# Performance work log

Measured on AMD Instinct MI355X. Metric: run time of the kernel, lower is better.

## Reference

```python
import jax, jax.numpy as jnp
import numpy as np

EPSILON = 0.01        # temperature
DIST_THRESH = 0.2
NUM_ITERS = 8         # sparse_rebalance_iters (== num_iters here)
TOPK = 64             # topk_support
NEG_INF = -1e9


def setup_inputs() -> dict:
    key = jax.random.key(0)
    k1, k2, k3 = jax.random.split(key, 3)
    B, N, M, D = 4, 4096, 4096, 128
    return {
        "source_feats": jax.random.normal(k1, (B, N, D), dtype=jnp.float32),
        "source_locs": jax.random.uniform(k2, (B, N, 2), dtype=jnp.float32),
        "target_locs": jax.random.uniform(k3, (B, M, 2), dtype=jnp.float32),
        "source_valid_mask": jnp.ones((B, N), dtype=bool),
        "target_valid_mask": jnp.ones((B, M), dtype=bool),
    }


def _sinkhorn_attn(source_locs, target_locs, source_valid_mask, target_valid_mask):
    # pairwise squared distances: [B, M, N]
    diff = target_locs[:, :, None, :] - source_locs[:, None, :, :]
    dist_sq = jnp.sum(diff * diff, axis=-1)
    log_k = -dist_sq / (EPSILON + 1e-8)
    valid = (dist_sq < DIST_THRESH ** 2)
    valid = valid & source_valid_mask[:, None, :] & target_valid_mask[:, :, None]

    B, M, N = valid.shape
    topk = min(TOPK, N)
    if topk < N:
        masked_log_k = jnp.where(valid, log_k, NEG_INF)
        _, topk_idx = jax.lax.top_k(masked_log_k, topk)  # [B, M, topk]
        support = jnp.zeros_like(valid).at[
            jnp.arange(B)[:, None, None], jnp.arange(M)[None, :, None], topk_idx
        ].set(True)
        valid = valid & support

    log_k = jnp.where(valid, log_k, NEG_INF)

    v = jnp.zeros((B, 1, N), dtype=log_k.dtype)
    u = jnp.zeros((B, M, 1), dtype=log_k.dtype)
    for _ in range(NUM_ITERS):
        u = -jax.nn.logsumexp(log_k + v, axis=2, keepdims=True)
        v = -jax.nn.logsumexp(log_k + u, axis=1, keepdims=True)
        v = jnp.where(source_valid_mask[:, None, :], v, 0.0)

    attn = jnp.exp(log_k + u + v)              # [B, M, N]
    has_source = valid.any(axis=-1, keepdims=True)  # [B, M, 1]
    return attn, has_source


def reference(source_feats, source_locs, target_locs, source_valid_mask, target_valid_mask):
    attn, has_source = _sinkhorn_attn(source_locs, target_locs,
                                      source_valid_mask, target_valid_mask)
    target_feats = jnp.einsum('bmn,bnd->bmd', attn, source_feats)
    target_feats = target_feats * target_valid_mask[:, :, None].astype(target_feats.dtype)
    target_feats = target_feats * has_source.astype(target_feats.dtype)
    return target_feats
```

## Files before the change

kernel.cpp:

```cpp
#include <hip/hip_runtime.h>
#include <math.h>

#define B 4
#define N 4096
#define M 4096
#define D 128
#define K 64
#define BT 256
#define WPB 4
#define RPW 4
#define CAP 768
#define CUTCAP 128
#define PC 128
#define EPS_DENOM 0.01000001f
#define THRESH2 0.04f
#define GC 16

__global__ __launch_bounds__(1024) void k_sort(const float* __restrict__ slocs,
        const float* __restrict__ tlocs,
        float4* __restrict__ sPack, float4* __restrict__ tPack,
        int* __restrict__ cellStart,
        int* __restrict__ colcnt, int* __restrict__ E, int* __restrict__ R,
        float* __restrict__ extraF, float* __restrict__ cs){
    __shared__ int hist[256], startS[256], fill[256], wtot[4];
    __shared__ float2 loc[N];
    __shared__ unsigned short scell[N];
    const int blk = blockIdx.x, tid = threadIdx.x;
    const bool tgt = blk >= B;
    const int b = tgt ? (blk - B) : blk;
    const int lane = tid & 63, w = tid >> 6;
    const float2* slp = (const float2*)((tgt ? tlocs : slocs) + (size_t)b * N * 2);
    float4* outPack = (tgt ? tPack : sPack) + (size_t)b * N;

    if (!tgt){
        for (int i = tid; i < N; i += 1024){
            colcnt[b * N + i] = 0;
            cs[b * N + i] = 1.0f;
        }
        if (b == 0){
            if (tid < B){ E[tid] = 0; R[tid] = 0; }
            if (tid < B * D) extraF[tid] = 0.f;
        }
    }

    if (tid < 256){ hist[tid] = 0; fill[tid] = 0; }
    __syncthreads();
    for (int i = tid; i < N; i += 1024){
        float2 p = slp[i];
        int cx = min(GC - 1, max(0, (int)(p.x * (float)GC)));
        int cy = min(GC - 1, max(0, (int)(p.y * (float)GC)));
        int cell = cy * GC + cx;
        loc[i] = p; scell[i] = (unsigned short)cell;
        atomicAdd(&hist[cell], 1);
    }
    __syncthreads();
    int hv = (tid < 256) ? hist[tid] : 0;
    int pre = hv;
    #pragma unroll
    for (int o = 1; o < 64; o <<= 1){ int t2 = __shfl_up(pre, o, 64); if (lane >= o) pre += t2; }
    if (tid < 256 && lane == 63) wtot[w] = pre;
    __syncthreads();
    if (tid < 256){
        int off = 0;
        for (int i = 0; i < w; ++i) off += wtot[i];
        int st = off + pre - hv;
        startS[tid] = st;
        if (!tgt) cellStart[b * 257 + tid] = st;
    }
    if (!tgt && tid == 0) cellStart[b * 257 + 256] = N;
    __syncthreads();
    for (int i = tid; i < N; i += 1024){
        int cell = scell[i];
        int pos = startS[cell] + atomicAdd(&fill[cell], 1);
        float2 p = loc[i];
        outPack[pos] = make_float4(p.x, p.y, __int_as_float(i), 0.f);
    }
}

__global__ __launch_bounds__(BT, 4) void k_build(const float4* __restrict__ sPack,
        const int* __restrict__ cellStart, const float4* __restrict__ tPack,
        float* __restrict__ elkA, int* __restrict__ idxA, int* __restrict__ cnt,
        int* __restrict__ colcnt, float* __restrict__ cscElk, int* __restrict__ cscRow,
        int* __restrict__ R){
    __shared__ int cs[257];
    __shared__ float cd2[WPB][CAP];
    __shared__ int   cn [WPB][CAP];
    __shared__ int   hist[WPB][64];
    __shared__ float cutd[WPB][CUTCAP];
    __shared__ int   cutn[WPB][CUTCAP];

    const int bid  = blockIdx.x;
    const int sb   = (bid & 7) * 128 + (bid >> 3);
    const int b    = sb >> 8;
    const int s00  = (sb & 255) * (WPB * RPW);
    const int tid  = threadIdx.x;
    const int w    = tid >> 6;
    const int lane = tid & 63;
    const unsigned long long pmask = (lane == 0) ? 0ull : ((1ull << lane) - 1);
    const float4* sp = sPack + (size_t)b * N;
    const float4* tp = tPack + (size_t)b * M;

    for (int i = tid; i < 257; i += BT) cs[i] = cellStart[b * 257 + i];
    __syncthreads();

    for (int r = 0; r < RPW; ++r){
        const int srt   = s00 + w * RPW + r;
        const float4 t  = tp[srt];
        const float tx  = t.x;
        const float ty  = t.y;
        const int m     = __float_as_int(t.z);
        const int rowid = b * M + m;

        hist[w][lane] = 0;

        const int cy0 = max(0, (int)floorf((ty - 0.2f) * (float)GC - 0.001f));
        const int cy1 = min(GC - 1, (int)floorf((ty + 0.2f) * (float)GC + 0.001f));

        int c = 0;
        for (int cy = cy0; cy <= cy1; ++cy){
            float rowLo = cy * 0.0625f, rowHi = rowLo + 0.0625f;
            float dymin = fmaxf(0.f, fmaxf(rowLo - ty, ty - rowHi));
            float dxm = sqrtf(fmaxf(THRESH2 - dymin * dymin + 1e-5f, 0.f));
            int cx0 = max(0, (int)floorf((tx - dxm) * (float)GC - 0.001f));
            int cx1 = min(GC - 1, (int)floorf((tx + dxm) * (float)GC + 0.001f));
            int s = cs[cy * GC + cx0], e = cs[cy * GC + cx1 + 1];
            for (int j0 = s; j0 < e; j0 += 64){
                int j = j0 + lane;
                bool valid = j < e;
                float d2 = 1e9f; int n = 0;
                if (valid){
                    float4 q = sp[j];
                    float dx = __fsub_rn(tx, q.x);
                    float dy = __fsub_rn(ty, q.y);
                    d2 = __fadd_rn(__fmul_rn(dx, dx), __fmul_rn(dy, dy));
                    n = __float_as_int(q.z);
                }
                bool in = valid && (d2 < THRESH2);
                unsigned long long ml = __ballot(in);
                if (in){
                    int p = c + __popcll(ml & pmask);
                    if (p < CAP){ cd2[w][p] = d2; cn[w][p] = n; }
                    atomicAdd(&hist[w][min((int)(d2 * 1600.0f), 63)], 1);
                }
                c += __popcll(ml);
            }
        }
        const int ctot = min(c, CAP);

        int h = hist[w][lane];
        int pre = h;
        #pragma unroll
        for (int o = 1; o < 64; o <<= 1){
            int t2 = __shfl_up(pre, o, 64);
            if (lane >= o) pre += t2;
        }
        int cutB = 64, q = 0;
        if (c > K){
            unsigned long long ge = __ballot(pre >= K);
            int fb = __ffsll((long long)ge) - 1;
            cutB = fb;
            q = K - __shfl(pre - h, fb, 64);
        }

        int base = 0, cutc = 0;
        for (int i0 = 0; i0 < ctot; i0 += 64){
            int i = i0 + lane;
            bool valid = i < ctot;
            float d2 = 1e9f; int n = 0;
            if (valid){ d2 = cd2[w][i]; n = cn[w][i]; }
            int bk = valid ? min((int)(d2 * 1600.0f), 63) : 64;
            bool low = valid && (bk < cutB);
            unsigned long long ml = __ballot(low);
            if (low){
                int p = base + __popcll(ml & pmask);
                float e = expf(-(d2 / EPS_DENOM));
                elkA[(size_t)rowid * K + p] = e;
                idxA[(size_t)rowid * K + p] = n;
                int bn = b * N + n;
                int slot = atomicAdd(&colcnt[bn], 1);
                if (slot < PC){
                    cscElk[(size_t)bn * PC + slot] = e;
                    cscRow[(size_t)bn * PC + slot] = rowid;
                }
            }
            base += __popcll(ml);
            if (cutB < 64){
                bool eq = valid && (bk == cutB);
                unsigned long long me = __ballot(eq);
                if (eq){
                    int p = cutc + __popcll(me & pmask);
                    if (p < CUTCAP){ cutd[w][p] = d2; cutn[w][p] = n; }
                }
                cutc += __popcll(me);
            }
        }

        if (c > K){
            int cc = min(cutc, CUTCAP);
            for (int i0 = 0; i0 < CUTCAP; i0 += 64){
                int i = i0 + lane;
                bool sel = false; float d2i = 0.f; int ni = 0;
                if (i < cc){
                    d2i = cutd[w][i]; ni = cutn[w][i];
                    int rank = 0;
                    for (int j = 0; j < cc; ++j){
                        float dj = cutd[w][j]; int nj = cutn[w][j];
                        rank += (dj < d2i) || (dj == d2i && nj < ni);
                    }
                    sel = rank < q;
                }
                unsigned long long ms = __ballot(sel);
                if (sel){
                    int p = base + __popcll(ms & pmask);
                    float e = expf(-(d2i / EPS_DENOM));
                    elkA[(size_t)rowid * K + p] = e;
                    idxA[(size_t)rowid * K + p] = ni;
                    int bn = b * N + ni;
                    int slot = atomicAdd(&colcnt[bn], 1);
                    if (slot < PC){
                        cscElk[(size_t)bn * PC + slot] = e;
                        cscRow[(size_t)bn * PC + slot] = rowid;
                    }
                }
                base += __popcll(ms);
                if (i0 + 64 >= cc) break;
            }
            if (lane == 0) cnt[rowid] = K;
        } else {
            if (lane == 0){
                cnt[rowid] = c;
                if (c == 0) atomicAdd(&R[b], 1);
            }
        }
    }
}

__global__ __launch_bounds__(256) void k_prep(const int* __restrict__ colcnt,
        int* __restrict__ E, const float* __restrict__ feats, float* __restrict__ extraF){
    int t = blockIdx.x * blockDim.x + threadIdx.x;
    int lane = t & 63, b = t >> 12;
    int cc = colcnt[t];
    unsigned long long em = __ballot(cc == 0);
    if (lane == 0 && em) atomicAdd(&E[b], __popcll(em));
    if (cc == 0){
        for (int d = 0; d < D; ++d)
            atomicAdd(&extraF[b * D + d], feats[(size_t)t * D + d]);
    }
}

__global__ __launch_bounds__(256) void kA(const float* __restrict__ elkA,
        const int* __restrict__ idxA, const int* __restrict__ cnt,
        const float* __restrict__ cs, const int* __restrict__ E, float* __restrict__ eu){
    int t = blockIdx.x * blockDim.x + threadIdx.x;
    int W = t >> 6, lane = t & 63;
    for (int rr = 0; rr < 4; ++rr){
        int rid = W * 4 + rr;
        int b = rid >> 12;
        int c = cnt[rid];
        float s = 0.f;
        if (lane < c){
            int ix = (b << 12) + idxA[(size_t)rid * K + lane];
            s = elkA[(size_t)rid * K + lane] / cs[ix];
        }
        #pragma unroll
        for (int o = 32; o; o >>= 1) s += __shfl_xor(s, o, 64);
        int Eb = E[b];
        if (c == 0 && Eb == 0){
            if (lane == 0) eu[rid] = 0.f;
        } else {
            if (Eb > 0) s += (float)Eb;
            if (lane == 0) eu[rid] = 1.0f / s;
        }
    }
}

__global__ __launch_bounds__(256) void kB(const float* __restrict__ cscElk,
        const int* __restrict__ cscRow, const int* __restrict__ colcnt,
        const float* __restrict__ eu, const int* __restrict__ R, float* __restrict__ cs){
    int t = blockIdx.x * blockDim.x + threadIdx.x;
    int W = t >> 6, lane = t & 63;
    for (int rr = 0; rr < 4; ++rr){
        int cid = W * 4 + rr;
        int b = cid >> 12;
        int cc = min(colcnt[cid], PC);
        float s = 0.f;
        for (int p = lane; p < cc; p += 64)
            s += cscElk[(size_t)cid * PC + p] * eu[cscRow[(size_t)cid * PC + p]];
        #pragma unroll
        for (int o = 32; o; o >>= 1) s += __shfl_xor(s, o, 64);
        if (lane == 0)
            cs[cid] = s + (float)R[b];
    }
}

__global__ __launch_bounds__(128) void k_out(const float* __restrict__ feats,
        const float* __restrict__ elkA, const int* __restrict__ idxA,
        const int* __restrict__ cnt, const float* __restrict__ eu,
        const float* __restrict__ cs, const float* __restrict__ extraF,
        float* __restrict__ out){
    __shared__ float att[K];
    __shared__ int   sidx[K];
    int rid = blockIdx.x;
    int b = rid >> 12;
    int tid = threadIdx.x;
    int c = cnt[rid];
    if (tid < K){
        float a = 0.f; int ix = 0;
        if (tid < c){
            ix = idxA[(size_t)rid * K + tid];
            a = elkA[(size_t)rid * K + tid] * eu[rid] / cs[(b << 12) + ix];
        }
        att[tid] = a; sidx[tid] = ix;
    }
    __syncthreads();
    float acc = 0.f;
    if (c > 0){
        acc = extraF[b * D + tid];
        for (int k = 0; k < c; ++k)
            acc += att[k] * feats[((size_t)((b << 12) + sidx[k])) * D + tid];
    }
    out[(size_t)rid * D + tid] = acc;
}

extern "C" void kernel_launch(void* const* d_in, const int* in_sizes, int n_in,
                              void* d_out, int out_size, void* d_ws, size_t ws_size,
                              hipStream_t stream){
    const float* feats = (const float*)d_in[0];
    const float* slocs = (const float*)d_in[1];
    const float* tlocs = (const float*)d_in[2];
    float* out = (float*)d_out;

    char* w = (char*)d_ws;
    size_t off = 0;
    auto carve = [&](size_t bytes) -> void* {
        void* p = w + off;
        off += (bytes + 255) & ~(size_t)255;
        return p;
    };
    float* elkA    = (float*)carve((size_t)B * M * K * 4);
    int*   idxA    = (int*)  carve((size_t)B * M * K * 4);
    float* cscElk  = (float*)carve((size_t)B * N * PC * 4);
    int*   cscRow  = (int*)  carve((size_t)B * N * PC * 4);
    int*   cnt     = (int*)  carve((size_t)B * M * 4);
    int*   colcnt  = (int*)  carve((size_t)B * N * 4);
    float* eu      = (float*)carve((size_t)B * M * 4);
    float* cs      = (float*)carve((size_t)B * N * 4);
    int*   E       = (int*)  carve(B * 4);
    int*   R       = (int*)  carve(B * 4);
    float* extraF  = (float*)carve((size_t)B * D * 4);
    float4* sPack  = (float4*)carve((size_t)B * N * 16);
    float4* tPack  = (float4*)carve((size_t)B * M * 16);
    int*   cellStart = (int*)carve((size_t)B * 257 * 4);

    k_sort<<<2 * B, 1024, 0, stream>>>(slocs, tlocs, sPack, tPack, cellStart,
                                       colcnt, E, R, extraF, cs);
    k_build<<<B * M / (WPB * RPW), BT, 0, stream>>>(sPack, cellStart, tPack,
            elkA, idxA, cnt, colcnt, cscElk, cscRow, R);
    k_prep<<<(B * N) / 256, 256, 0, stream>>>(colcnt, E, feats, extraF);
    for (int it = 0; it < 8; ++it){
        kA<<<B * M / 16, 256, 0, stream>>>(elkA, idxA, cnt, cs, E, eu);
        kB<<<B * N / 16, 256, 0, stream>>>(cscElk, cscRow, colcnt, eu, R, cs);
    }
    k_out<<<B * M, D, 0, stream>>>(feats, elkA, idxA, cnt, eu, cs, extraF, out);
}
```

Before: 259.0 us.

## Stage shared source candidates in LDS per block and spatially order output rows

k_build now computes the union bounding region of the block's 16 target rows, loads those source points once into shared memory as compact xy plus id, and stores only 16-bit local indices per candidate, recomputing distances in the second pass instead of storing d2 and n. This cuts repeated global float4 loads across the four rows in each wave and across waves, and also cuts LDS footprint. k_out remaps blocks through the spatially sorted target order with an XCD-aware swizzle, so neighbouring blocks gather overlapping source feature rows and get better cache reuse. The cost is extra syncs, a fallback path when the region exceeds SCAP, and a dependent tPack load in k_out.

Result: no change. 259.0 us (-0.0%).

```diff
diff --git a/kernel.cpp b/kernel.cpp
--- a/kernel.cpp
+++ b/kernel.cpp
@@ -12,6 +12,7 @@
 #define CAP 768
 #define CUTCAP 128
 #define PC 128
+#define SCAP 2048
 #define EPS_DENOM 0.01000001f
 #define THRESH2 0.04f
 #define GC 16
@@ -83,11 +84,15 @@
         int* __restrict__ colcnt, float* __restrict__ cscElk, int* __restrict__ cscRow,
         int* __restrict__ R){
     __shared__ int cs[257];
-    __shared__ float cd2[WPB][CAP];
-    __shared__ int   cn [WPB][CAP];
+    __shared__ float2 sxy[SCAP];
+    __shared__ int    sid[SCAP];
+    __shared__ unsigned short cj[WPB][CAP];
     __shared__ int   hist[WPB][64];
     __shared__ float cutd[WPB][CUTCAP];
     __shared__ int   cutn[WPB][CUTCAP];
+    __shared__ float4 rowT[16];
+    __shared__ int gB[16], gL[16], lB[16];
+    __shared__ int stot;
 
     const int bid  = blockIdx.x;
     const int sb   = (bid & 7) * 128 + (bid >> 3);
@@ -101,11 +106,54 @@
     const float4* tp = tPack + (size_t)b * M;
 
     for (int i = tid; i < 257; i += BT) cs[i] = cellStart[b * 257 + i];
+    if (tid < 16) rowT[tid] = tp[s00 + tid];
+    __syncthreads();
+
+    float txmin = 1e9f, txmax = -1e9f, tymin = 1e9f, tymax = -1e9f;
+    #pragma unroll
+    for (int i = 0; i < 16; ++i){
+        float4 t = rowT[i];
+        txmin = fminf(txmin, t.x); txmax = fmaxf(txmax, t.x);
+        tymin = fminf(tymin, t.y); tymax = fmaxf(tymax, t.y);
+    }
+    const int bcy0 = max(0, (int)floorf((tymin - 0.2f) * (float)GC - 0.001f));
+    const int bcy1 = min(GC - 1, (int)floorf((tymax + 0.2f) * (float)GC + 0.001f));
+    const int ncy  = bcy1 - bcy0 + 1;
+    if (tid < ncy && tid < 16){
+        int cy = bcy0 + tid;
+        float rowLo = cy * 0.0625f, rowHi = rowLo + 0.0625f;
+        float dymin = fmaxf(0.f, fmaxf(rowLo - tymax, tymin - rowHi));
+        float dxm = sqrtf(fmaxf(THRESH2 - dymin * dymin + 1e-5f, 0.f));
+        int cx0 = max(0, (int)floorf((txmin - dxm) * (float)GC - 0.001f));
+        int cx1 = min(GC - 1, (int)floorf((txmax + dxm) * (float)GC + 0.001f));
+        int s = cs[cy * GC + cx0], e = cs[cy * GC + cx1 + 1];
+        gB[tid] = s; gL[tid] = e - s;
+    }
+    __syncthreads();
+    if (tid == 0){
+        if (ncy > 16) stot = SCAP + 1;
+        else {
+            int acc = 0;
+            for (int i = 0; i < ncy; ++i){ lB[i] = acc; acc += gL[i]; }
+            stot = acc;
+        }
+    }
+    __syncthreads();
+    const bool staged = (stot <= SCAP);
+    if (staged){
+        for (int i = 0; i < ncy; ++i){
+            int s = gB[i], len = gL[i], l0 = lB[i];
+            for (int j = tid; j < len; j += BT){
+                float4 q = sp[s + j];
+                sxy[l0 + j] = make_float2(q.x, q.y);
+                sid[l0 + j] = __float_as_int(q.z);
+            }
+        }
+    }
     __syncthreads();
 
     for (int r = 0; r < RPW; ++r){
-        const int srt   = s00 + w * RPW + r;
-        const float4 t  = tp[srt];
+        const float4 t  = rowT[w * RPW + r];
         const float tx  = t.x;
         const float ty  = t.y;
         const int m     = __float_as_int(t.z);
@@ -124,22 +172,26 @@
             int cx0 = max(0, (int)floorf((tx - dxm) * (float)GC - 0.001f));
             int cx1 = min(GC - 1, (int)floorf((tx + dxm) * (float)GC + 0.001f));
             int s = cs[cy * GC + cx0], e = cs[cy * GC + cx1 + 1];
-            for (int j0 = s; j0 < e; j0 += 64){
-                int j = j0 + lane;
-                bool valid = j < e;
-                float d2 = 1e9f; int n = 0;
+            int len = e - s;
+            int base_l = staged ? (lB[cy - bcy0] + (s - gB[cy - bcy0])) : s;
+            for (int j0 = 0; j0 < len; j0 += 64){
+                int i = j0 + lane;
+                bool valid = i < len;
+                int lp = base_l + i;
+                float d2 = 1e9f;
                 if (valid){
-                    float4 q = sp[j];
-                    float dx = __fsub_rn(tx, q.x);
-                    float dy = __fsub_rn(ty, q.y);
+                    float qx, qy;
+                    if (staged){ float2 q = sxy[lp]; qx = q.x; qy = q.y; }
+                    else       { float4 q = sp[lp];  qx = q.x; qy = q.y; }
+                    float dx = __fsub_rn(tx, qx);
+                    float dy = __fsub_rn(ty, qy);
                     d2 = __fadd_rn(__fmul_rn(dx, dx), __fmul_rn(dy, dy));
-                    n = __float_as_int(q.z);
                 }
                 bool in = valid && (d2 < THRESH2);
                 unsigned long long ml = __ballot(in);
                 if (in){
                     int p = c + __popcll(ml & pmask);
-                    if (p < CAP){ cd2[w][p] = d2; cn[w][p] = n; }
+                    if (p < CAP) cj[w][p] = (unsigned short)lp;
                     atomicAdd(&hist[w][min((int)(d2 * 1600.0f), 63)], 1);
                 }
                 c += __popcll(ml);
@@ -167,7 +219,15 @@
             int i = i0 + lane;
             bool valid = i < ctot;
             float d2 = 1e9f; int n = 0;
-            if (valid){ d2 = cd2[w][i]; n = cn[w][i]; }
+            if (valid){
+                int lp = cj[w][i];
+                float qx, qy;
+                if (staged){ float2 q = sxy[lp]; qx = q.x; qy = q.y; n = sid[lp]; }
+                else       { float4 q = sp[lp];  qx = q.x; qy = q.y; n = __float_as_int(q.z); }
+                float dx = __fsub_rn(tx, qx);
+                float dy = __fsub_rn(ty, qy);
+                d2 = __fadd_rn(__fmul_rn(dx, dx), __fmul_rn(dy, dy));
+            }
             int bk = valid ? min((int)(d2 * 1600.0f), 63) : 64;
             bool low = valid && (bk < cutB);
             unsigned long long ml = __ballot(low);
@@ -297,11 +357,15 @@
         const float* __restrict__ elkA, const int* __restrict__ idxA,
         const int* __restrict__ cnt, const float* __restrict__ eu,
         const float* __restrict__ cs, const float* __restrict__ extraF,
-        float* __restrict__ out){
+        const float4* __restrict__ tPack, float* __restrict__ out){
     __shared__ float att[K];
     __shared__ int   sidx[K];
-    int rid = blockIdx.x;
-    int b = rid >> 12;
+    int bid = blockIdx.x;
+    int sg  = (bid & 7) * 2048 + (bid >> 3);
+    int b   = sg >> 12;
+    int srt = sg & 4095;
+    int m   = __float_as_int(tPack[(size_t)b * M + srt].z);
+    int rid = (b << 12) + m;
     int tid = threadIdx.x;
     int c = cnt[rid];
     if (tid < K){
@@ -361,5 +425,5 @@
         kA<<<B * M / 16, 256, 0, stream>>>(elkA, idxA, cnt, cs, E, eu);
         kB<<<B * N / 16, 256, 0, stream>>>(cscElk, cscRow, colcnt, eu, R, cs);
     }
-    k_out<<<B * M, D, 0, stream>>>(feats, elkA, idxA, cnt, eu, cs, extraF, out);
-}
+    k_out<<<B * M, D, 0, stream>>>(feats, elkA, idxA, cnt, eu, cs, extraF, tPack, out);
+}
```
